# Kernel tuning notes

Measured on AMD Instinct MI355X. Metric: run time of the kernel, lower is better.

Reference implementation:

```python
import jax, jax.numpy as jnp
import numpy as np

DIST_THRESHOLD = 3.33  # threshold on SQUARED distances (pytorch3d knn_points.dists are squared)


def setup_inputs() -> dict:
    key = jax.random.key(0)
    k1, k2, k3, k4, k5, k6 = jax.random.split(key, 6)
    B, N, D = 4, 8192, 3
    points_src = jax.random.normal(k1, (B, N, D), dtype=jnp.float32)
    points_dst = jax.random.normal(k2, (B, N, D), dtype=jnp.float32)
    flows_pred = jax.random.normal(k3, (B, N, D), dtype=jnp.float32)
    flows_gt = jax.random.normal(k4, (B, N, D), dtype=jnp.float32)
    masks_src = jax.random.randint(k5, (B, N), 0, 2, dtype=jnp.int32)
    masks_dst = jax.random.randint(k6, (B, N), 0, 2, dtype=jnp.int32)
    return {"points_src": points_src, "points_dst": points_dst,
            "flows_pred": flows_pred, "flows_gt": flows_gt,
            "masks_src": masks_src, "masks_dst": masks_dst}


def _pairwise_sq_dists(a, b):
    # a: [N,3], b: [M,3] -> [N,M] squared euclidean distances via gram trick
    a2 = jnp.sum(a * a, axis=-1)  # [N]
    b2 = jnp.sum(b * b, axis=-1)  # [M]
    d2 = a2[:, None] + b2[None, :] - 2.0 * (a @ b.T)
    return jnp.maximum(d2, 0.0)


def _chamfer_thresholded(pw, pd, ms, md):
    # pw: warped src points [N,3]; pd: dst points [M,3]; ms/md: validity masks (>0)
    valid_s = ms > 0  # [N]
    valid_d = md > 0  # [M]
    d2 = _pairwise_sq_dists(pw, pd)  # [N,M]
    # K=1 NN in each direction; invalid points in the *search* set get +inf
    d_wt = jnp.min(jnp.where(valid_d[None, :], d2, jnp.inf), axis=1)  # [N]
    d_tw = jnp.min(jnp.where(valid_s[:, None], d2, jnp.inf), axis=0)  # [M]
    # thresholded mean over valid query points (mirrors boolean-index + .mean())
    sel_wt = valid_s & (d_wt < DIST_THRESHOLD)
    sel_tw = valid_d & (d_tw < DIST_THRESHOLD)
    mean_wt = jnp.sum(jnp.where(sel_wt, d_wt, 0.0)) / jnp.sum(sel_wt)
    mean_tw = jnp.sum(jnp.where(sel_tw, d_tw, 0.0)) / jnp.sum(sel_tw)
    return mean_wt + mean_tw


def reference(points_src, points_dst, flows_pred, flows_gt, masks_src, masks_dst):
    points_src_warped = points_src + flows_pred  # [B,N,3]
    per_sample = jax.vmap(_chamfer_thresholded)(points_src_warped, points_dst,
                                                masks_src, masks_dst)  # [B]
    return jnp.sum(per_sample)
```

## Files before the change

### kernel.cpp

```cpp
#include <hip/hip_runtime.h>
#include <hip/hip_bf16.h>

#define NPTS 8192
#define NB   4
#define BLK  256
#define RAWC 1024
#define NQC  (NPTS / RAWC)
#define NSL  16
#define SRAW (NPTS / NSL)
#define THR  3.33f

#define OFF_PART 16384

__device__ __forceinline__ void load_pt(int side, int g,
    const float* __restrict__ Ps, const float* __restrict__ Pd,
    const float* __restrict__ F,  const int* __restrict__ Ms,
    const int* __restrict__ Md,
    float& x, float& y, float& z, bool& v)
{
    if (side == 0) {
        x = Ps[3*g+0] + F[3*g+0];
        y = Ps[3*g+1] + F[3*g+1];
        z = Ps[3*g+2] + F[3*g+2];
        v = Ms[g] > 0;
    } else {
        x = Pd[3*g+0]; y = Pd[3*g+1]; z = Pd[3*g+2];
        v = Md[g] > 0;
    }
}

template<int KMAX>
__device__ __forceinline__ void inner_loop(const float4* __restrict__ sp, int sd,
                                           const float4* __restrict__ qb, int nd,
                                           float* __restrict__ pb, int tid)
{
    float qx[KMAX], qy[KMAX], qz[KMAX], bt[KMAX];
#pragma unroll
    for (int k = 0; k < KMAX; ++k) {
        const int q = k * BLK + tid;
        const float4 p = qb[q < nd ? q : 0];
        qx[k] = p.x; qy[k] = p.y; qz[k] = p.z;
        bt[k] = -1e30f;
    }
#pragma unroll 4
    for (int j = 0; j < sd; ++j) {
        const float4 s = sp[j];
#pragma unroll
        for (int k = 0; k < KMAX; ++k) {
            float t = fmaf(qx[k], s.x, s.w);
            t = fmaf(qy[k], s.y, t);
            t = fmaf(qz[k], s.z, t);
            bt[k] = fmaxf(bt[k], t);
        }
    }
#pragma unroll
    for (int k = 0; k < KMAX; ++k) {
        const int q = k * BLK + tid;
        if (q < nd) pb[q] = bt[k];
    }
}

__global__ __launch_bounds__(BLK) void knn_kernel(
    const float* __restrict__ Ps, const float* __restrict__ Pd,
    const float* __restrict__ F,  const int* __restrict__ Ms,
    const int* __restrict__ Md,   float* __restrict__ part,
    unsigned* __restrict__ ctl)
{
    const int b = blockIdx.z, dir = blockIdx.y;
    const int qc = blockIdx.x / NSL, sl = blockIdx.x % NSL;
    const int tid = threadIdx.x, lane = tid & 63, w = tid >> 6;
    const int qi = b * 2 + dir;

    if (blockIdx.x == 0 && dir == 0 && b == 0)
        for (int i = tid; i < 512; i += BLK) ctl[i] = 0;

    __shared__ float4 qb[RAWC];
    __shared__ float4 sp[SRAW];
    __shared__ int wcq[4], wcs[4], cnt_s[2];

    float qxr[4], qyr[4], qzr[4]; bool qvr[4];
#pragma unroll
    for (int r = 0; r < 4; ++r) {
        const int g = b * NPTS + qc * RAWC + r * BLK + tid;
        load_pt(dir, g, Ps, Pd, F, Ms, Md, qxr[r], qyr[r], qzr[r], qvr[r]);
    }
    float sxr[2], syr[2], szr[2]; bool svr[2];
#pragma unroll
    for (int r = 0; r < 2; ++r) {
        const int g = b * NPTS + sl * SRAW + r * BLK + tid;
        load_pt(1 - dir, g, Ps, Pd, F, Ms, Md, sxr[r], syr[r], szr[r], svr[r]);
    }

    const int cq = (int)qvr[0] + qvr[1] + qvr[2] + qvr[3];
    const int cs = (int)svr[0] + svr[1];
    int pq = cq, ps = cs;
#pragma unroll
    for (int o = 1; o < 64; o <<= 1) {
        int t1 = __shfl_up(pq, o), t2 = __shfl_up(ps, o);
        if (lane >= o) { pq += t1; ps += t2; }
    }
    if (lane == 63) { wcq[w] = pq; wcs[w] = ps; }
    __syncthreads();
    int bq = 0, bs = 0;
#pragma unroll
    for (int i = 0; i < 4; ++i) if (i < w) { bq += wcq[i]; bs += wcs[i]; }
    int oq = bq + pq - cq;
    int os = bs + ps - cs;
#pragma unroll
    for (int r = 0; r < 4; ++r)
        if (qvr[r]) { qb[oq] = make_float4(qxr[r], qyr[r], qzr[r], 0.f); ++oq; }
#pragma unroll
    for (int r = 0; r < 2; ++r)
        if (svr[r]) {
            sp[os] = make_float4(2.f * sxr[r], 2.f * syr[r], 2.f * szr[r],
                                 -(sxr[r]*sxr[r] + syr[r]*syr[r] + szr[r]*szr[r]));
            ++os;
        }
    if (tid == BLK - 1) { cnt_s[0] = bq + pq; cnt_s[1] = bs + ps; }
    __syncthreads();
    const int nd = cnt_s[0], sd = cnt_s[1];

    float* pb = part + ((size_t)qi * NSL + sl) * NPTS + qc * RAWC;
    switch ((nd + BLK - 1) >> 8) {
        case 1: inner_loop<1>(sp, sd, qb, nd, pb, tid); break;
        case 2: inner_loop<2>(sp, sd, qb, nd, pb, tid); break;
        case 3: inner_loop<3>(sp, sd, qb, nd, pb, tid); break;
        case 4: inner_loop<4>(sp, sd, qb, nd, pb, tid); break;
        default: break;
    }
}

__global__ __launch_bounds__(BLK) void final_kernel(
    const float* __restrict__ Ps, const float* __restrict__ Pd,
    const float* __restrict__ F,  const int* __restrict__ Ms,
    const int* __restrict__ Md,   const float* __restrict__ part,
    unsigned* __restrict__ ctl,   float* __restrict__ out)
{
    const int b = blockIdx.z, dir = blockIdx.y, qc = blockIdx.x;
    const int tid = threadIdx.x, lane = tid & 63, w = tid >> 6;
    const int qi = b * 2 + dir;

    __shared__ float q2b[RAWC];
    __shared__ int wcq[4], nd_s;

    float qxr[4], qyr[4], qzr[4]; bool qvr[4];
#pragma unroll
    for (int r = 0; r < 4; ++r) {
        const int g = b * NPTS + qc * RAWC + r * BLK + tid;
        load_pt(dir, g, Ps, Pd, F, Ms, Md, qxr[r], qyr[r], qzr[r], qvr[r]);
    }
    const int cq = (int)qvr[0] + qvr[1] + qvr[2] + qvr[3];
    int pq = cq;
#pragma unroll
    for (int o = 1; o < 64; o <<= 1) {
        int t1 = __shfl_up(pq, o);
        if (lane >= o) pq += t1;
    }
    if (lane == 63) wcq[w] = pq;
    __syncthreads();
    int bq = 0;
#pragma unroll
    for (int i = 0; i < 4; ++i) if (i < w) bq += wcq[i];
    int oq = bq + pq - cq;
#pragma unroll
    for (int r = 0; r < 4; ++r)
        if (qvr[r]) {
            q2b[oq] = fmaf(qxr[r], qxr[r], fmaf(qyr[r], qyr[r], qzr[r] * qzr[r]));
            ++oq;
        }
    if (tid == BLK - 1) nd_s = bq + pq;
    __syncthreads();
    const int nd = nd_s;

    const float* pp = part + (size_t)qi * NSL * NPTS + qc * RAWC;
    float s = 0.f, c = 0.f;
    for (int dq = tid; dq < nd; dq += BLK) {
        float m = -1e30f;
#pragma unroll
        for (int sl = 0; sl < NSL; ++sl)
            m = fmaxf(m, pp[(size_t)sl * NPTS + dq]);
        const float dd = fmaxf(q2b[dq] - m, 0.f);
        if (dd < THR) { s += dd; c += 1.f; }
    }
#pragma unroll
    for (int off = 32; off; off >>= 1) {
        s += __shfl_down(s, off);
        c += __shfl_down(c, off);
    }
    __shared__ float red[8];
    if (lane == 0) { red[w] = s; red[4 + w] = c; }
    __syncthreads();
    if (tid == 0) {
        float* psum  = (float*)(ctl + 1024);
        float* pcnt  = (float*)(ctl + 1152);
        float* meanv = (float*)(ctl + 288);
        psum[qi * NQC + qc] = red[0] + red[1] + red[2] + red[3];
        pcnt[qi * NQC + qc] = red[4] + red[5] + red[6] + red[7];
        const unsigned r = __hip_atomic_fetch_add(&ctl[qi * 32], 1u,
                              __ATOMIC_ACQ_REL, __HIP_MEMORY_SCOPE_AGENT);
        if (r == NQC - 1) {
            float S = 0.f, C = 0.f;
            for (int g = 0; g < NQC; ++g) {
                S += psum[qi * NQC + g];
                C += pcnt[qi * NQC + g];
            }
            meanv[qi] = S / C;
            const unsigned r2 = __hip_atomic_fetch_add(&ctl[256], 1u,
                                   __ATOMIC_ACQ_REL, __HIP_MEMORY_SCOPE_AGENT);
            if (r2 == 2 * NB - 1) {
                float a = 0.f;
#pragma unroll
                for (int i = 0; i < 2 * NB; ++i) a += meanv[i];
                out[0] = a;
            }
        }
    }
}

extern "C" void kernel_launch(void* const* d_in, const int* in_sizes, int n_in,
                              void* d_out, int out_size, void* d_ws, size_t ws_size,
                              hipStream_t stream)
{
    const float* Ps = (const float*)d_in[0];
    const float* Pd = (const float*)d_in[1];
    const float* F  = (const float*)d_in[2];
    const int* Ms = (const int*)d_in[4];
    const int* Md = (const int*)d_in[5];
    float* out = (float*)d_out;

    unsigned* ctl = (unsigned*)d_ws;
    float* part = (float*)((char*)d_ws + OFF_PART);

    knn_kernel<<<dim3(NQC * NSL, 2, NB), BLK, 0, stream>>>(
        Ps, Pd, F, Ms, Md, part, ctl);

    final_kernel<<<dim3(NQC, 2, NB), BLK, 0, stream>>>(
        Ps, Pd, F, Ms, Md, part, ctl, out);
}
```

Baseline: 30.64 us.

## Add global compaction pass and split kNN over dense valid points

Adds a compaction kernel that packs the valid points of each cloud into a dense global array along with their squared norms. The kNN kernel then tiles over valid points only, with 32 source slices and query chunks of the dense set, so blocks no longer carry per-chunk masking imbalance and blocks past the valid count exit early. The final kernel reads the precomputed norms. This costs an extra kernel launch and a serial compaction over 8 blocks, and it doubles the partial-result traffic because there are more slices.

```diff
diff --git a/kernel.cpp b/kernel.cpp
--- a/kernel.cpp
+++ b/kernel.cpp
@@ -3,14 +3,21 @@
 
 #define NPTS 8192
 #define NB   4
+#define NQI  8
 #define BLK  256
-#define RAWC 1024
-#define NQC  (NPTS / RAWC)
-#define NSL  16
-#define SRAW (NPTS / NSL)
+#define CH   1024
+#define NCH  8
+#define NSL  32
+#define LMAX 256
 #define THR  3.33f
 
-#define OFF_PART 16384
+#define W_T2    256
+#define W_MEAN  288
+#define W_PSUM  320
+#define W_PCNT  384
+#define W_NCNT  448
+#define OFF_PART  4096
+#define OFF_DENSE (4096 + (size_t)NQI * NSL * NPTS * 4)
 
 __device__ __forceinline__ void load_pt(int side, int g,
     const float* __restrict__ Ps, const float* __restrict__ Pd,
@@ -29,188 +36,167 @@
     }
 }
 
-template<int KMAX>
-__device__ __forceinline__ void inner_loop(const float4* __restrict__ sp, int sd,
-                                           const float4* __restrict__ qb, int nd,
-                                           float* __restrict__ pb, int tid)
-{
-    float qx[KMAX], qy[KMAX], qz[KMAX], bt[KMAX];
-#pragma unroll
-    for (int k = 0; k < KMAX; ++k) {
-        const int q = k * BLK + tid;
-        const float4 p = qb[q < nd ? q : 0];
+__global__ __launch_bounds__(BLK) void compact_kernel(
+    const float* __restrict__ Ps, const float* __restrict__ Pd,
+    const float* __restrict__ F,  const int* __restrict__ Ms,
+    const int* __restrict__ Md,   float4* __restrict__ dense,
+    unsigned* __restrict__ ctl)
+{
+    const int qi = blockIdx.x, b = qi >> 1, side = qi & 1;
+    const int tid = threadIdx.x, lane = tid & 63, w = tid >> 6;
+    __shared__ int wc[4];
+
+    if (qi == 0)
+        for (int i = tid; i < 320; i += BLK) ctl[i] = 0;
+
+    int carry = 0;
+    for (int rnd = 0; rnd < 4; ++rnd) {
+        float xx[8], yy[8], zz[8]; bool vv[8];
+#pragma unroll
+        for (int r = 0; r < 8; ++r) {
+            const int g = b * NPTS + rnd * 2048 + r * BLK + tid;
+            load_pt(side, g, Ps, Pd, F, Ms, Md, xx[r], yy[r], zz[r], vv[r]);
+        }
+        int c = 0;
+#pragma unroll
+        for (int r = 0; r < 8; ++r) c += vv[r];
+        int p = c;
+#pragma unroll
+        for (int o = 1; o < 64; o <<= 1) {
+            int t = __shfl_up(p, o);
+            if (lane >= o) p += t;
+        }
+        if (lane == 63) wc[w] = p;
+        __syncthreads();
+        int base = carry + (p - c);
+        int total = 0;
+#pragma unroll
+        for (int i = 0; i < 4; ++i) {
+            if (i < w) base += wc[i];
+            total += wc[i];
+        }
+#pragma unroll
+        for (int r = 0; r < 8; ++r)
+            if (vv[r]) {
+                dense[(size_t)qi * NPTS + base] =
+                    make_float4(xx[r], yy[r], zz[r],
+                        fmaf(xx[r], xx[r], fmaf(yy[r], yy[r], zz[r] * zz[r])));
+                ++base;
+            }
+        carry += total;
+        __syncthreads();
+    }
+    if (tid == 0) ctl[W_NCNT + qi] = (unsigned)carry;
+}
+
+__global__ __launch_bounds__(BLK) void knn_kernel(
+    const float4* __restrict__ dense, const unsigned* __restrict__ ctl,
+    float* __restrict__ part)
+{
+    const int b = blockIdx.z, dir = blockIdx.y;
+    const int qc = blockIdx.x / NSL, sl = blockIdx.x % NSL;
+    const int qi = b * 2 + dir, si = qi ^ 1;
+    const int tid = threadIdx.x;
+
+    const int nq = (int)ctl[W_NCNT + qi];
+    const int ns = (int)ctl[W_NCNT + si];
+    if (qc * CH >= nq) return;
+    const int L = (ns + NSL - 1) / NSL;
+    const int start = sl * L;
+    int len = ns - start; if (len > L) len = L;
+    if (len <= 0) return;
+
+    __shared__ float4 sp[LMAX];
+    if (tid < len) {
+        const float4 p = dense[(size_t)si * NPTS + start + tid];
+        sp[tid] = make_float4(2.f * p.x, 2.f * p.y, 2.f * p.z, -p.w);
+    }
+    __syncthreads();
+
+    float qx[4], qy[4], qz[4], bt[4]; bool qv[4];
+#pragma unroll
+    for (int k = 0; k < 4; ++k) {
+        const int q = qc * CH + k * BLK + tid;
+        qv[k] = q < nq;
+        const float4 p = dense[(size_t)qi * NPTS + (qv[k] ? q : 0)];
         qx[k] = p.x; qy[k] = p.y; qz[k] = p.z;
         bt[k] = -1e30f;
     }
+
 #pragma unroll 4
-    for (int j = 0; j < sd; ++j) {
+    for (int j = 0; j < len; ++j) {
         const float4 s = sp[j];
 #pragma unroll
-        for (int k = 0; k < KMAX; ++k) {
+        for (int k = 0; k < 4; ++k) {
             float t = fmaf(qx[k], s.x, s.w);
             t = fmaf(qy[k], s.y, t);
             t = fmaf(qz[k], s.z, t);
             bt[k] = fmaxf(bt[k], t);
         }
     }
-#pragma unroll
-    for (int k = 0; k < KMAX; ++k) {
-        const int q = k * BLK + tid;
-        if (q < nd) pb[q] = bt[k];
-    }
-}
-
-__global__ __launch_bounds__(BLK) void knn_kernel(
-    const float* __restrict__ Ps, const float* __restrict__ Pd,
-    const float* __restrict__ F,  const int* __restrict__ Ms,
-    const int* __restrict__ Md,   float* __restrict__ part,
-    unsigned* __restrict__ ctl)
-{
-    const int b = blockIdx.z, dir = blockIdx.y;
-    const int qc = blockIdx.x / NSL, sl = blockIdx.x % NSL;
+
+    float* pb = part + ((size_t)qi * NSL + sl) * NPTS;
+#pragma unroll
+    for (int k = 0; k < 4; ++k)
+        if (qv[k]) pb[qc * CH + k * BLK + tid] = bt[k];
+}
+
+__global__ __launch_bounds__(BLK) void final_kernel(
+    const float4* __restrict__ dense, const float* __restrict__ part,
+    unsigned* __restrict__ ctl, float* __restrict__ out)
+{
+    const int b = blockIdx.z, dir = blockIdx.y, qc = blockIdx.x;
+    const int qi = b * 2 + dir;
     const int tid = threadIdx.x, lane = tid & 63, w = tid >> 6;
-    const int qi = b * 2 + dir;
-
-    if (blockIdx.x == 0 && dir == 0 && b == 0)
-        for (int i = tid; i < 512; i += BLK) ctl[i] = 0;
-
-    __shared__ float4 qb[RAWC];
-    __shared__ float4 sp[SRAW];
-    __shared__ int wcq[4], wcs[4], cnt_s[2];
-
-    float qxr[4], qyr[4], qzr[4]; bool qvr[4];
-#pragma unroll
-    for (int r = 0; r < 4; ++r) {
-        const int g = b * NPTS + qc * RAWC + r * BLK + tid;
-        load_pt(dir, g, Ps, Pd, F, Ms, Md, qxr[r], qyr[r], qzr[r], qvr[r]);
-    }
-    float sxr[2], syr[2], szr[2]; bool svr[2];
-#pragma unroll
-    for (int r = 0; r < 2; ++r) {
-        const int g = b * NPTS + sl * SRAW + r * BLK + tid;
-        load_pt(1 - dir, g, Ps, Pd, F, Ms, Md, sxr[r], syr[r], szr[r], svr[r]);
-    }
-
-    const int cq = (int)qvr[0] + qvr[1] + qvr[2] + qvr[3];
-    const int cs = (int)svr[0] + svr[1];
-    int pq = cq, ps = cs;
-#pragma unroll
-    for (int o = 1; o < 64; o <<= 1) {
-        int t1 = __shfl_up(pq, o), t2 = __shfl_up(ps, o);
-        if (lane >= o) { pq += t1; ps += t2; }
-    }
-    if (lane == 63) { wcq[w] = pq; wcs[w] = ps; }
-    __syncthreads();
-    int bq = 0, bs = 0;
-#pragma unroll
-    for (int i = 0; i < 4; ++i) if (i < w) { bq += wcq[i]; bs += wcs[i]; }
-    int oq = bq + pq - cq;
-    int os = bs + ps - cs;
-#pragma unroll
-    for (int r = 0; r < 4; ++r)
-        if (qvr[r]) { qb[oq] = make_float4(qxr[r], qyr[r], qzr[r], 0.f); ++oq; }
-#pragma unroll
-    for (int r = 0; r < 2; ++r)
-        if (svr[r]) {
-            sp[os] = make_float4(2.f * sxr[r], 2.f * syr[r], 2.f * szr[r],
-                                 -(sxr[r]*sxr[r] + syr[r]*syr[r] + szr[r]*szr[r]));
-            ++os;
-        }
-    if (tid == BLK - 1) { cnt_s[0] = bq + pq; cnt_s[1] = bs + ps; }
-    __syncthreads();
-    const int nd = cnt_s[0], sd = cnt_s[1];
-
-    float* pb = part + ((size_t)qi * NSL + sl) * NPTS + qc * RAWC;
-    switch ((nd + BLK - 1) >> 8) {
-        case 1: inner_loop<1>(sp, sd, qb, nd, pb, tid); break;
-        case 2: inner_loop<2>(sp, sd, qb, nd, pb, tid); break;
-        case 3: inner_loop<3>(sp, sd, qb, nd, pb, tid); break;
-        case 4: inner_loop<4>(sp, sd, qb, nd, pb, tid); break;
-        default: break;
-    }
-}
-
-__global__ __launch_bounds__(BLK) void final_kernel(
-    const float* __restrict__ Ps, const float* __restrict__ Pd,
-    const float* __restrict__ F,  const int* __restrict__ Ms,
-    const int* __restrict__ Md,   const float* __restrict__ part,
-    unsigned* __restrict__ ctl,   float* __restrict__ out)
-{
-    const int b = blockIdx.z, dir = blockIdx.y, qc = blockIdx.x;
-    const int tid = threadIdx.x, lane = tid & 63, w = tid >> 6;
-    const int qi = b * 2 + dir;
-
-    __shared__ float q2b[RAWC];
-    __shared__ int wcq[4], nd_s;
-
-    float qxr[4], qyr[4], qzr[4]; bool qvr[4];
-#pragma unroll
-    for (int r = 0; r < 4; ++r) {
-        const int g = b * NPTS + qc * RAWC + r * BLK + tid;
-        load_pt(dir, g, Ps, Pd, F, Ms, Md, qxr[r], qyr[r], qzr[r], qvr[r]);
-    }
-    const int cq = (int)qvr[0] + qvr[1] + qvr[2] + qvr[3];
-    int pq = cq;
-#pragma unroll
-    for (int o = 1; o < 64; o <<= 1) {
-        int t1 = __shfl_up(pq, o);
-        if (lane >= o) pq += t1;
-    }
-    if (lane == 63) wcq[w] = pq;
-    __syncthreads();
-    int bq = 0;
-#pragma unroll
-    for (int i = 0; i < 4; ++i) if (i < w) bq += wcq[i];
-    int oq = bq + pq - cq;
-#pragma unroll
-    for (int r = 0; r < 4; ++r)
-        if (qvr[r]) {
-            q2b[oq] = fmaf(qxr[r], qxr[r], fmaf(qyr[r], qyr[r], qzr[r] * qzr[r]));
-            ++oq;
-        }
-    if (tid == BLK - 1) nd_s = bq + pq;
-    __syncthreads();
-    const int nd = nd_s;
-
-    const float* pp = part + (size_t)qi * NSL * NPTS + qc * RAWC;
+    __shared__ float red[8];
+
+    const int nq = (int)ctl[W_NCNT + qi];
     float s = 0.f, c = 0.f;
-    for (int dq = tid; dq < nd; dq += BLK) {
-        float m = -1e30f;
-#pragma unroll
-        for (int sl = 0; sl < NSL; ++sl)
-            m = fmaxf(m, pp[(size_t)sl * NPTS + dq]);
-        const float dd = fmaxf(q2b[dq] - m, 0.f);
-        if (dd < THR) { s += dd; c += 1.f; }
+    if (qc * CH < nq) {
+        const float* pr = part + (size_t)qi * NSL * NPTS;
+#pragma unroll
+        for (int k = 0; k < 4; ++k) {
+            const int q = qc * CH + k * BLK + tid;
+            if (q < nq) {
+                float m = -1e30f;
+#pragma unroll
+                for (int sl = 0; sl < NSL; ++sl)
+                    m = fmaxf(m, pr[(size_t)sl * NPTS + q]);
+                const float qw = dense[(size_t)qi * NPTS + q].w;
+                const float dd = fmaxf(qw - m, 0.f);
+                if (dd < THR) { s += dd; c += 1.f; }
+            }
+        }
     }
 #pragma unroll
     for (int off = 32; off; off >>= 1) {
         s += __shfl_down(s, off);
         c += __shfl_down(c, off);
     }
-    __shared__ float red[8];
     if (lane == 0) { red[w] = s; red[4 + w] = c; }
     __syncthreads();
     if (tid == 0) {
-        float* psum  = (float*)(ctl + 1024);
-        float* pcnt  = (float*)(ctl + 1152);
-        float* meanv = (float*)(ctl + 288);
-        psum[qi * NQC + qc] = red[0] + red[1] + red[2] + red[3];
-        pcnt[qi * NQC + qc] = red[4] + red[5] + red[6] + red[7];
-        const unsigned r = __hip_atomic_fetch_add(&ctl[qi * 32], 1u,
-                              __ATOMIC_ACQ_REL, __HIP_MEMORY_SCOPE_AGENT);
-        if (r == NQC - 1) {
+        float* psum  = (float*)(ctl + W_PSUM);
+        float* pcnt  = (float*)(ctl + W_PCNT);
+        float* meanv = (float*)(ctl + W_MEAN);
+        psum[qi * NCH + qc] = red[0] + red[1] + red[2] + red[3];
+        pcnt[qi * NCH + qc] = red[4] + red[5] + red[6] + red[7];
+        const unsigned r1 = __hip_atomic_fetch_add(&ctl[qi * 32], 1u,
+                               __ATOMIC_ACQ_REL, __HIP_MEMORY_SCOPE_AGENT);
+        if (r1 == NCH - 1) {
             float S = 0.f, C = 0.f;
-            for (int g = 0; g < NQC; ++g) {
-                S += psum[qi * NQC + g];
-                C += pcnt[qi * NQC + g];
+#pragma unroll
+            for (int g = 0; g < NCH; ++g) {
+                S += psum[qi * NCH + g];
+                C += pcnt[qi * NCH + g];
             }
             meanv[qi] = S / C;
-            const unsigned r2 = __hip_atomic_fetch_add(&ctl[256], 1u,
+            const unsigned r2 = __hip_atomic_fetch_add(&ctl[W_T2], 1u,
                                    __ATOMIC_ACQ_REL, __HIP_MEMORY_SCOPE_AGENT);
-            if (r2 == 2 * NB - 1) {
+            if (r2 == NQI - 1) {
                 float a = 0.f;
 #pragma unroll
-                for (int i = 0; i < 2 * NB; ++i) a += meanv[i];
+                for (int i = 0; i < NQI; ++i) a += meanv[i];
                 out[0] = a;
             }
         }
@@ -230,10 +216,11 @@
 
     unsigned* ctl = (unsigned*)d_ws;
     float* part = (float*)((char*)d_ws + OFF_PART);
-
-    knn_kernel<<<dim3(NQC * NSL, 2, NB), BLK, 0, stream>>>(
-        Ps, Pd, F, Ms, Md, part, ctl);
-
-    final_kernel<<<dim3(NQC, 2, NB), BLK, 0, stream>>>(
-        Ps, Pd, F, Ms, Md, part, ctl, out);
-}
+    float4* dense = (float4*)((char*)d_ws + OFF_DENSE);
+
+    compact_kernel<<<dim3(NQI), BLK, 0, stream>>>(Ps, Pd, F, Ms, Md, dense, ctl);
+
+    knn_kernel<<<dim3(NCH * NSL, 2, NB), BLK, 0, stream>>>(dense, ctl, part);
+
+    final_kernel<<<dim3(NCH, 2, NB), BLK, 0, stream>>>(dense, part, ctl, out);
+}
```

Measured after the change: 47.70 us. 1.56x slower.
